# Performance work log

Hardware: AMD Instinct MI355X
Metric: run time of the kernel (lower is better)

The kernel has to match this reference:

```python
import jax, jax.numpy as jnp
import numpy as np

B, S, D, H = 4, 2048, 1024, 16
DH = D // H  # 64
EPS = 1e-5


def setup_inputs() -> dict:
    key = jax.random.key(0)
    ks = jax.random.split(key, 6)
    scale = 0.02
    return {
        "x": jax.random.normal(ks[0], (B, S, D), dtype=jnp.float32),
        "Wq": jax.random.normal(ks[1], (H, D, DH), dtype=jnp.float32) * scale,
        "Wk": jax.random.normal(ks[2], (H, D, DH), dtype=jnp.float32) * scale,
        "Wv": jax.random.normal(ks[3], (H, D, DH), dtype=jnp.float32) * scale,
        "Wo": jax.random.normal(ks[4], (D, D), dtype=jnp.float32) * scale,
        "bo": jnp.zeros((D,), dtype=jnp.float32),
        "gamma": jnp.ones((D,), dtype=jnp.float32),
        "beta": jnp.zeros((D,), dtype=jnp.float32),
    }


def reference(x, Wq, Wk, Wv, Wo, bo, gamma, beta):
    # Per-head projections, stacked across heads: [B,H,S,DH]
    q = jnp.einsum("bsd,hdk->bhsk", x, Wq)
    k = jnp.einsum("bsd,hdk->bhsk", x, Wk)
    v = jnp.einsum("bsd,hdk->bhsk", x, Wv)
    inv_scale = 1.0 / jnp.sqrt(jnp.float32(DH))  # key.size(-1) == head_dim
    scores = jnp.einsum("bhqk,bhsk->bhqs", q, k) * inv_scale  # [B,H,S,S]
    attn = jax.nn.softmax(scores, axis=-1)
    ctx = jnp.einsum("bhqs,bhsk->bhqk", attn, v)  # [B,H,S,DH]
    # concat heads -> [B,S,D]
    concat = jnp.transpose(ctx, (0, 2, 1, 3)).reshape(B, S, D)
    proj = concat @ Wo + bo  # fc_out (Wo stored as [in,out])
    added = proj + x  # residual add
    mu = jnp.mean(added, axis=-1, keepdims=True)
    var = jnp.mean(jnp.square(added - mu), axis=-1, keepdims=True)
    normed = (added - mu) * jax.lax.rsqrt(var + EPS)
    return normed * gamma + beta
```

## Files before the change

### kernel.cpp

```cpp
#include <hip/hip_runtime.h>
#include <hip/hip_bf16.h>
#include <stdint.h>

#define DEV __device__ __forceinline__

typedef short s16x8 __attribute__((ext_vector_type(8)));
typedef float f32x4 __attribute__((ext_vector_type(4)));

DEV void async_load16(const void* g, void* l) {
  __builtin_amdgcn_global_load_lds((void __attribute__((address_space(1)))*)(g),
                                   (void __attribute__((address_space(3)))*)(l),
                                   16, 0, 0);
}

__global__ __launch_bounds__(256) void cast_x_kernel(const float* __restrict__ in,
                                                     __hip_bfloat16* __restrict__ out, int n4) {
  int i = blockIdx.x * 256 + threadIdx.x;
  if (i >= n4) return;
  float4 v = ((const float4*)in)[i];
  alignas(8) __hip_bfloat16 t[4] = {__float2bfloat16(v.x), __float2bfloat16(v.y),
                                    __float2bfloat16(v.z), __float2bfloat16(v.w)};
  *(uint2*)(out + (size_t)i * 4) = *(const uint2*)t;
}

__global__ __launch_bounds__(256) void transpose_cast_kernel(const float* __restrict__ src,
                                                             __hip_bfloat16* __restrict__ dst,
                                                             int R, int C, float scale) {
  __shared__ float tile[64][65];
  const int r0 = blockIdx.x * 64, c0 = blockIdx.y * 64, bt = blockIdx.z;
  const int tc = threadIdx.x & 63, tr = threadIdx.x >> 6;
  const float* sp = src + (size_t)bt * R * C;
#pragma unroll
  for (int rr = 0; rr < 64; rr += 4)
    tile[tr + rr][tc] = sp[(size_t)(r0 + tr + rr) * C + c0 + tc];
  __syncthreads();
  __hip_bfloat16* dp = dst + (size_t)bt * R * C;
#pragma unroll
  for (int rr = 0; rr < 64; rr += 4) {
    int cc = tr + rr;
    dp[(size_t)(c0 + cc) * R + r0 + tc] = __float2bfloat16(tile[tc][cc] * scale);
  }
}

template <int MODE>
__global__ __launch_bounds__(256) void gemm128(const __hip_bfloat16* __restrict__ A,
                                               const __hip_bfloat16* __restrict__ Bt,
                                               void* __restrict__ out0,
                                               void* __restrict__ out1,
                                               const float* __restrict__ bias,
                                               const float* __restrict__ resid,
                                               int M, int N, int K) {
  __shared__ __hip_bfloat16 As[128 * 32];
  __shared__ __hip_bfloat16 Bs[128 * 32];
  const int tid = threadIdx.x;
  const int lane = tid & 63, w = tid >> 6;
  const int lr = lane & 15, lq = lane >> 4;
  const int wm = w >> 1, wn = w & 1;
  const int m0 = blockIdx.y * 128, n0 = blockIdx.x * 128;

  const f32x4 fz = {0.f, 0.f, 0.f, 0.f};
  f32x4 acc[4][4];
#pragma unroll
  for (int i = 0; i < 4; i++)
#pragma unroll
    for (int j = 0; j < 4; j++) acc[i][j] = fz;

  const int kiters = K >> 5;
  for (int kt = 0; kt < kiters; kt++) {
    __syncthreads();
#pragma unroll
    for (int r = 0; r < 2; r++) {
      const int c = r * 256 + tid;
      const int row = c >> 2, kc = c & 3;
      async_load16((const short*)A + (size_t)(m0 + row) * K + kt * 32 + kc * 8,
                   (char*)As + (r * 256 + (tid & 0xC0)) * 16);
      async_load16((const short*)Bt + (size_t)(n0 + row) * K + kt * 32 + kc * 8,
                   (char*)Bs + (r * 256 + (tid & 0xC0)) * 16);
    }
    __syncthreads();
    const short* Ap = (const short*)As;
    const short* Bp = (const short*)Bs;
    s16x8 av[4], bv[4];
#pragma unroll
    for (int i = 0; i < 4; i++)
      av[i] = *(const s16x8*)(Ap + (wm * 64 + i * 16 + lr) * 32 + lq * 8);
#pragma unroll
    for (int j = 0; j < 4; j++)
      bv[j] = *(const s16x8*)(Bp + (wn * 64 + j * 16 + lr) * 32 + lq * 8);
#pragma unroll
    for (int i = 0; i < 4; i++)
#pragma unroll
      for (int j = 0; j < 4; j++)
        acc[i][j] = __builtin_amdgcn_mfma_f32_16x16x32_bf16(av[i], bv[j], acc[i][j], 0, 0, 0);
  }

  __hip_bfloat16* dst01 = nullptr;
  if constexpr (MODE == 0) dst01 = (__hip_bfloat16*)((n0 < 1024) ? out0 : out1);

#pragma unroll
  for (int i = 0; i < 4; i++)
#pragma unroll
    for (int j = 0; j < 4; j++)
#pragma unroll
      for (int r = 0; r < 4; r++) {
        const int row = m0 + wm * 64 + i * 16 + lq * 4 + r;
        const int col = n0 + wn * 64 + j * 16 + lr;
        const float v = acc[i][j][r];
        if constexpr (MODE == 0) {
          const int bb = row >> 11, s = row & 2047;
          const int colq = col & 1023;
          dst01[((((size_t)bb * 16 + (colq >> 6)) * 2048 + s) << 6) + (col & 63)] =
              __float2bfloat16(v);
        } else if constexpr (MODE == 1) {
          const int bb = col >> 11, s = col & 2047;
          ((__hip_bfloat16*)out0)[(size_t)bb * 2097152 + (size_t)row * 2048 + s] =
              __float2bfloat16(v);
        } else {
          const size_t idx = (size_t)row * 1024 + col;
          ((float*)out0)[idx] = v + bias[col] + resid[idx];
        }
      }
}

__global__ __launch_bounds__(256, 4) void flash_kernel(const __hip_bfloat16* __restrict__ Qg,
                                                       const __hip_bfloat16* __restrict__ Kg,
                                                       const __hip_bfloat16* __restrict__ Vtg,
                                                       __hip_bfloat16* __restrict__ Og) {
  __shared__ __hip_bfloat16 Klds[128 * 64];
  __shared__ __hip_bfloat16 Vlds[64 * 128];
  __shared__ __hip_bfloat16 Plds[64 * 64];
  const int tid = threadIdx.x;
  const int lane = tid & 63, w = tid >> 6;
  const int lr = lane & 15, lq = lane >> 4;
  const int qt = blockIdx.x, h = blockIdx.y, b = blockIdx.z;
  const size_t bh = (size_t)b * 16 + h;
  const short* Qbase = (const short*)Qg + (bh * 2048 + (size_t)qt * 128) * 64;
  const short* Kbh = (const short*)Kg + bh * 2048 * 64;
  const short* Vbh = (const short*)Vtg + bh * 64 * 2048;

  s16x8 qb[2][2];
#pragma unroll
  for (int nt = 0; nt < 2; nt++)
#pragma unroll
    for (int ks = 0; ks < 2; ks++)
      qb[nt][ks] = *(const s16x8*)(Qbase + (w * 32 + nt * 16 + lr) * 64 + ks * 32 + lq * 8);

  const f32x4 fz = {0.f, 0.f, 0.f, 0.f};
  f32x4 o[2][4];
#pragma unroll
  for (int mt = 0; mt < 2; mt++)
#pragma unroll
    for (int nt = 0; nt < 4; nt++) o[mt][nt] = fz;
  float lsum[2] = {0.f, 0.f};

  for (int kb = 0; kb < 16; kb++) {
    __syncthreads();
    const short* Ksrc = Kbh + kb * 128 * 64;
#pragma unroll
    for (int r = 0; r < 4; r++) {
      int c = r * 256 + tid;
      int row = c >> 3, ck = c & 7;
      async_load16(Ksrc + row * 64 + (ck ^ (row & 7)) * 8,
                   (char*)Klds + (r * 256 + (tid & 0xC0)) * 16);
    }
#pragma unroll
    for (int r = 0; r < 4; r++) {
      int c = r * 256 + tid;
      int row = c >> 4, ck = c & 15;
      async_load16(Vbh + (size_t)row * 2048 + kb * 128 + (ck ^ (row & 15)) * 8,
                   (char*)Vlds + (r * 256 + (tid & 0xC0)) * 16);
    }
    __syncthreads();

    const short* Kp = (const short*)Klds;
    const short* Vp = (const short*)Vlds;
    short* Pp = (short*)Plds;

#pragma unroll
    for (int c = 0; c < 4; c++) {
      s16x8 kf[2][2];
#pragma unroll
      for (int mt = 0; mt < 2; mt++)
#pragma unroll
        for (int ks = 0; ks < 2; ks++) {
          int kvrow = c * 32 + mt * 16 + lr;
          kf[mt][ks] = *(const s16x8*)(Kp + kvrow * 64 + ((ks * 4 + lq) ^ (kvrow & 7)) * 8);
        }
      f32x4 st[2][2];
#pragma unroll
      for (int mt = 0; mt < 2; mt++)
#pragma unroll
        for (int nt = 0; nt < 2; nt++) st[mt][nt] = fz;
#pragma unroll
      for (int mt = 0; mt < 2; mt++)
#pragma unroll
        for (int ks = 0; ks < 2; ks++)
#pragma unroll
          for (int nt = 0; nt < 2; nt++)
            st[mt][nt] =
                __builtin_amdgcn_mfma_f32_16x16x32_bf16(kf[mt][ks], qb[nt][ks], st[mt][nt], 0, 0, 0);

#pragma unroll
      for (int mt = 0; mt < 2; mt++)
#pragma unroll
        for (int nt = 0; nt < 2; nt++) {
          float e0 = __expf(st[mt][nt][0]);
          float e1 = __expf(st[mt][nt][1]);
          float e2 = __expf(st[mt][nt][2]);
          float e3 = __expf(st[mt][nt][3]);
          lsum[nt] += (e0 + e1) + (e2 + e3);
          int q = w * 32 + nt * 16 + lr;
          int p = q >> 1, u = q & 1;
          int lineChunk = u * 4 + mt * 2 + (lq >> 1);
          int addr = p * 64 + ((lineChunk ^ (p & 7)) << 3) + (lq & 1) * 4;
          alignas(8) __hip_bfloat16 t4[4] = {__float2bfloat16(e0), __float2bfloat16(e1),
                                             __float2bfloat16(e2), __float2bfloat16(e3)};
          *(uint2*)(Pp + addr) = *(const uint2*)t4;
        }

      s16x8 pa[2];
#pragma unroll
      for (int mt = 0; mt < 2; mt++) {
        int q = w * 32 + mt * 16 + lr;
        int p = q >> 1, u = q & 1;
        pa[mt] = *(const s16x8*)(Pp + p * 64 + (((u * 4 + lq) ^ (p & 7)) << 3));
      }
#pragma unroll
      for (int nt = 0; nt < 4; nt++) {
        int vrow = nt * 16 + lr;
        s16x8 vb = *(const s16x8*)(Vp + vrow * 128 + (((c * 4 + lq) ^ (vrow & 15)) << 3));
        o[0][nt] = __builtin_amdgcn_mfma_f32_16x16x32_bf16(pa[0], vb, o[0][nt], 0, 0, 0);
        o[1][nt] = __builtin_amdgcn_mfma_f32_16x16x32_bf16(pa[1], vb, o[1][nt], 0, 0, 0);
      }
    }
  }

#pragma unroll
  for (int nt = 0; nt < 2; nt++) {
    lsum[nt] += __shfl_xor(lsum[nt], 16);
    lsum[nt] += __shfl_xor(lsum[nt], 32);
  }

#pragma unroll
  for (int mt = 0; mt < 2; mt++)
#pragma unroll
    for (int r = 0; r < 4; r++) {
      float lv = __shfl(lsum[mt], lq * 4 + r);
      float inv = 1.0f / lv;
      int rowg = qt * 128 + w * 32 + mt * 16 + lq * 4 + r;
#pragma unroll
      for (int nt = 0; nt < 4; nt++) {
        Og[((size_t)b * 2048 + rowg) * 1024 + h * 64 + nt * 16 + lr] =
            __float2bfloat16(o[mt][nt][r] * inv);
      }
    }
}

__global__ __launch_bounds__(256) void ln_kernel(const float* __restrict__ tmp,
                                                 const float* __restrict__ gamma,
                                                 const float* __restrict__ beta,
                                                 float* __restrict__ out) {
  const int row = blockIdx.x, tid = threadIdx.x;
  const int lane = tid & 63, w = tid >> 6;
  const float* rp = tmp + (size_t)row * 1024;
  float4 v = ((const float4*)rp)[tid];
  float s = v.x + v.y + v.z + v.w;
  float ss = v.x * v.x + v.y * v.y + v.z * v.z + v.w * v.w;
#pragma unroll
  for (int off = 32; off >= 1; off >>= 1) {
    s += __shfl_xor(s, off);
    ss += __shfl_xor(ss, off);
  }
  __shared__ float red[8];
  if (lane == 0) {
    red[w] = s;
    red[4 + w] = ss;
  }
  __syncthreads();
  s = red[0] + red[1] + red[2] + red[3];
  ss = red[4] + red[5] + red[6] + red[7];
  const float mu = s * (1.0f / 1024.0f);
  const float var = ss * (1.0f / 1024.0f) - mu * mu;
  const float rstd = rsqrtf(var + 1e-5f);
  float4 g = ((const float4*)gamma)[tid];
  float4 be = ((const float4*)beta)[tid];
  float4 ov;
  ov.x = (v.x - mu) * rstd * g.x + be.x;
  ov.y = (v.y - mu) * rstd * g.y + be.y;
  ov.z = (v.z - mu) * rstd * g.z + be.z;
  ov.w = (v.w - mu) * rstd * g.w + be.w;
  ((float4*)(out + (size_t)row * 1024))[tid] = ov;
}

extern "C" void kernel_launch(void* const* d_in, const int* in_sizes, int n_in,
                              void* d_out, int out_size, void* d_ws, size_t ws_size,
                              hipStream_t stream) {
  (void)in_sizes; (void)n_in; (void)out_size; (void)ws_size;
  const float* x = (const float*)d_in[0];
  const float* Wq = (const float*)d_in[1];
  const float* Wk = (const float*)d_in[2];
  const float* Wv = (const float*)d_in[3];
  const float* Wo = (const float*)d_in[4];
  const float* bo = (const float*)d_in[5];
  const float* gamma = (const float*)d_in[6];
  const float* beta = (const float*)d_in[7];
  float* out = (float*)d_out;
  char* ws = (char*)d_ws;

  __hip_bfloat16* xb = (__hip_bfloat16*)(ws + 0);
  __hip_bfloat16* wqT = (__hip_bfloat16*)(ws + 16777216);
  __hip_bfloat16* wkT = (__hip_bfloat16*)(ws + 18874368);
  __hip_bfloat16* wvT = (__hip_bfloat16*)(ws + 20971520);
  __hip_bfloat16* woT = (__hip_bfloat16*)(ws + 23068672);
  __hip_bfloat16* Q = (__hip_bfloat16*)(ws + 25165824);
  __hip_bfloat16* Kt = (__hip_bfloat16*)(ws + 41943040);
  __hip_bfloat16* Vt = (__hip_bfloat16*)(ws + 58720256);
  __hip_bfloat16* cc = (__hip_bfloat16*)(ws + 75497472);
  float* tmp = (float*)(ws + 25165824);

  cast_x_kernel<<<8192, 256, 0, stream>>>(x, xb, 2097152);
  transpose_cast_kernel<<<dim3(16, 1, 16), 256, 0, stream>>>(Wq, wqT, 1024, 64, 0.125f);
  transpose_cast_kernel<<<dim3(16, 1, 16), 256, 0, stream>>>(Wk, wkT, 1024, 64, 1.0f);
  transpose_cast_kernel<<<dim3(16, 1, 16), 256, 0, stream>>>(Wv, wvT, 1024, 64, 1.0f);
  transpose_cast_kernel<<<dim3(16, 16, 1), 256, 0, stream>>>(Wo, woT, 1024, 1024, 1.0f);

  gemm128<0><<<dim3(16, 64), 256, 0, stream>>>(xb, wqT, Q, Kt, nullptr, nullptr, 8192, 2048, 1024);
  gemm128<1><<<dim3(64, 8), 256, 0, stream>>>(wvT, xb, Vt, nullptr, nullptr, nullptr, 1024, 8192, 1024);

  flash_kernel<<<dim3(16, 16, 4), 256, 0, stream>>>(Q, Kt, Vt, cc);

  gemm128<2><<<dim3(8, 64), 256, 0, stream>>>(cc, woT, tmp, nullptr, bo, x, 8192, 1024, 1024);
  ln_kernel<<<8192, 256, 0, stream>>>(tmp, gamma, beta, out);
}
```

Before: 330.8 us.

## Keep softmax probabilities in registers and enlarge flash query tile to 256

The flash kernel now builds the P operand directly in registers. It permutes the K rows so the score MFMA output layout matches the A-operand layout of the PV MFMA, which removes the LDS round trip for P. Each block now covers 256 query rows (64 per wave), halving K/V loads per query, and the grid is reordered so the head/batch index varies fastest. The log2(e) factor is folded into the Q weight scale so exp2 and rcp intrinsics replace expf and division. The cost is roughly doubled accumulator registers, which drops occupancy to 2 blocks per CU, and a grid of only 512 blocks.

```diff
diff --git a/kernel.cpp b/kernel.cpp
--- a/kernel.cpp
+++ b/kernel.cpp
@@ -6,11 +6,19 @@
 
 typedef short s16x8 __attribute__((ext_vector_type(8)));
 typedef float f32x4 __attribute__((ext_vector_type(4)));
+typedef int i32x4 __attribute__((ext_vector_type(4)));
 
 DEV void async_load16(const void* g, void* l) {
   __builtin_amdgcn_global_load_lds((void __attribute__((address_space(1)))*)(g),
                                    (void __attribute__((address_space(3)))*)(l),
                                    16, 0, 0);
+}
+
+DEV unsigned pack_bf16x2(float a, float b) {
+  __hip_bfloat162 h = __float22bfloat162_rn(make_float2(a, b));
+  union { __hip_bfloat162 h2; unsigned u; } cv;
+  cv.h2 = h;
+  return cv.u;
 }
 
 __global__ __launch_bounds__(256) void cast_x_kernel(const float* __restrict__ in,
@@ -122,36 +130,39 @@
       }
 }
 
-__global__ __launch_bounds__(256, 4) void flash_kernel(const __hip_bfloat16* __restrict__ Qg,
+__global__ __launch_bounds__(256, 2) void flash_kernel(const __hip_bfloat16* __restrict__ Qg,
                                                        const __hip_bfloat16* __restrict__ Kg,
                                                        const __hip_bfloat16* __restrict__ Vtg,
                                                        __hip_bfloat16* __restrict__ Og) {
   __shared__ __hip_bfloat16 Klds[128 * 64];
   __shared__ __hip_bfloat16 Vlds[64 * 128];
-  __shared__ __hip_bfloat16 Plds[64 * 64];
   const int tid = threadIdx.x;
   const int lane = tid & 63, w = tid >> 6;
   const int lr = lane & 15, lq = lane >> 4;
-  const int qt = blockIdx.x, h = blockIdx.y, b = blockIdx.z;
+  const int hb = blockIdx.x, qt = blockIdx.y;
+  const int h = hb >> 2, b = hb & 3;
   const size_t bh = (size_t)b * 16 + h;
-  const short* Qbase = (const short*)Qg + (bh * 2048 + (size_t)qt * 128) * 64;
+  const short* Qbase = (const short*)Qg + (bh * 2048 + (size_t)qt * 256) * 64;
   const short* Kbh = (const short*)Kg + bh * 2048 * 64;
   const short* Vbh = (const short*)Vtg + bh * 64 * 2048;
 
-  s16x8 qb[2][2];
-#pragma unroll
-  for (int nt = 0; nt < 2; nt++)
+  const int rbase = (lr >> 2) * 8 + (lr & 3);
+  const int gk = (lr & 3) | (((lr >> 2) & 1) << 2);
+
+  s16x8 qb[4][2];
+#pragma unroll
+  for (int nt = 0; nt < 4; nt++)
 #pragma unroll
     for (int ks = 0; ks < 2; ks++)
-      qb[nt][ks] = *(const s16x8*)(Qbase + (w * 32 + nt * 16 + lr) * 64 + ks * 32 + lq * 8);
+      qb[nt][ks] = *(const s16x8*)(Qbase + (w * 64 + nt * 16 + lr) * 64 + ks * 32 + lq * 8);
 
   const f32x4 fz = {0.f, 0.f, 0.f, 0.f};
-  f32x4 o[2][4];
-#pragma unroll
-  for (int mt = 0; mt < 2; mt++)
-#pragma unroll
-    for (int nt = 0; nt < 4; nt++) o[mt][nt] = fz;
-  float lsum[2] = {0.f, 0.f};
+  f32x4 o[4][4];
+#pragma unroll
+  for (int i = 0; i < 4; i++)
+#pragma unroll
+    for (int j = 0; j < 4; j++) o[i][j] = fz;
+  float lsum[4] = {0.f, 0.f, 0.f, 0.f};
 
   for (int kb = 0; kb < 16; kb++) {
     __syncthreads();
@@ -160,7 +171,8 @@
     for (int r = 0; r < 4; r++) {
       int c = r * 256 + tid;
       int row = c >> 3, ck = c & 7;
-      async_load16(Ksrc + row * 64 + (ck ^ (row & 7)) * 8,
+      int g = (row & 3) | (((row >> 3) & 1) << 2);
+      async_load16(Ksrc + row * 64 + (ck ^ g) * 8,
                    (char*)Klds + (r * 256 + (tid & 0xC0)) * 16);
     }
 #pragma unroll
@@ -174,84 +186,59 @@
 
     const short* Kp = (const short*)Klds;
     const short* Vp = (const short*)Vlds;
-    short* Pp = (short*)Plds;
 
 #pragma unroll
     for (int c = 0; c < 4; c++) {
-      s16x8 kf[2][2];
-#pragma unroll
-      for (int mt = 0; mt < 2; mt++)
-#pragma unroll
-        for (int ks = 0; ks < 2; ks++) {
-          int kvrow = c * 32 + mt * 16 + lr;
-          kf[mt][ks] = *(const s16x8*)(Kp + kvrow * 64 + ((ks * 4 + lq) ^ (kvrow & 7)) * 8);
+      union { i32x4 i; s16x8 s; } pa[4];
+
+#pragma unroll
+      for (int mt = 0; mt < 2; mt++) {
+        const int kvrow = c * 32 + mt * 4 + rbase;
+        s16x8 kf0 = *(const s16x8*)(Kp + kvrow * 64 + ((0 * 4 + lq) ^ gk) * 8);
+        s16x8 kf1 = *(const s16x8*)(Kp + kvrow * 64 + ((1 * 4 + lq) ^ gk) * 8);
+#pragma unroll
+        for (int nt = 0; nt < 4; nt++) {
+          f32x4 st = fz;
+          st = __builtin_amdgcn_mfma_f32_16x16x32_bf16(kf0, qb[nt][0], st, 0, 0, 0);
+          st = __builtin_amdgcn_mfma_f32_16x16x32_bf16(kf1, qb[nt][1], st, 0, 0, 0);
+          float e0 = __builtin_amdgcn_exp2f(st[0]);
+          float e1 = __builtin_amdgcn_exp2f(st[1]);
+          float e2 = __builtin_amdgcn_exp2f(st[2]);
+          float e3 = __builtin_amdgcn_exp2f(st[3]);
+          lsum[nt] += (e0 + e1) + (e2 + e3);
+          pa[nt].i[mt * 2 + 0] = (int)pack_bf16x2(e0, e1);
+          pa[nt].i[mt * 2 + 1] = (int)pack_bf16x2(e2, e3);
         }
-      f32x4 st[2][2];
-#pragma unroll
-      for (int mt = 0; mt < 2; mt++)
-#pragma unroll
-        for (int nt = 0; nt < 2; nt++) st[mt][nt] = fz;
-#pragma unroll
-      for (int mt = 0; mt < 2; mt++)
-#pragma unroll
-        for (int ks = 0; ks < 2; ks++)
-#pragma unroll
-          for (int nt = 0; nt < 2; nt++)
-            st[mt][nt] =
-                __builtin_amdgcn_mfma_f32_16x16x32_bf16(kf[mt][ks], qb[nt][ks], st[mt][nt], 0, 0, 0);
-
-#pragma unroll
-      for (int mt = 0; mt < 2; mt++)
-#pragma unroll
-        for (int nt = 0; nt < 2; nt++) {
-          float e0 = __expf(st[mt][nt][0]);
-          float e1 = __expf(st[mt][nt][1]);
-          float e2 = __expf(st[mt][nt][2]);
-          float e3 = __expf(st[mt][nt][3]);
-          lsum[nt] += (e0 + e1) + (e2 + e3);
-          int q = w * 32 + nt * 16 + lr;
-          int p = q >> 1, u = q & 1;
-          int lineChunk = u * 4 + mt * 2 + (lq >> 1);
-          int addr = p * 64 + ((lineChunk ^ (p & 7)) << 3) + (lq & 1) * 4;
-          alignas(8) __hip_bfloat16 t4[4] = {__float2bfloat16(e0), __float2bfloat16(e1),
-                                             __float2bfloat16(e2), __float2bfloat16(e3)};
-          *(uint2*)(Pp + addr) = *(const uint2*)t4;
-        }
-
-      s16x8 pa[2];
-#pragma unroll
-      for (int mt = 0; mt < 2; mt++) {
-        int q = w * 32 + mt * 16 + lr;
-        int p = q >> 1, u = q & 1;
-        pa[mt] = *(const s16x8*)(Pp + p * 64 + (((u * 4 + lq) ^ (p & 7)) << 3));
       }
-#pragma unroll
-      for (int nt = 0; nt < 4; nt++) {
-        int vrow = nt * 16 + lr;
-        s16x8 vb = *(const s16x8*)(Vp + vrow * 128 + (((c * 4 + lq) ^ (vrow & 15)) << 3));
-        o[0][nt] = __builtin_amdgcn_mfma_f32_16x16x32_bf16(pa[0], vb, o[0][nt], 0, 0, 0);
-        o[1][nt] = __builtin_amdgcn_mfma_f32_16x16x32_bf16(pa[1], vb, o[1][nt], 0, 0, 0);
+
+#pragma unroll
+      for (int ndh = 0; ndh < 4; ndh++) {
+        int vrow = ndh * 16 + lr;
+        s16x8 vb = *(const s16x8*)(Vp + vrow * 128 + (((c * 4 + lq) ^ lr) << 3));
+#pragma unroll
+        for (int nt = 0; nt < 4; nt++)
+          o[nt][ndh] = __builtin_amdgcn_mfma_f32_16x16x32_bf16(pa[nt].s, vb, o[nt][ndh], 0, 0, 0);
       }
     }
   }
 
 #pragma unroll
-  for (int nt = 0; nt < 2; nt++) {
+  for (int nt = 0; nt < 4; nt++) {
     lsum[nt] += __shfl_xor(lsum[nt], 16);
     lsum[nt] += __shfl_xor(lsum[nt], 32);
   }
 
 #pragma unroll
-  for (int mt = 0; mt < 2; mt++)
+  for (int nt = 0; nt < 4; nt++)
 #pragma unroll
     for (int r = 0; r < 4; r++) {
-      float lv = __shfl(lsum[mt], lq * 4 + r);
-      float inv = 1.0f / lv;
-      int rowg = qt * 128 + w * 32 + mt * 16 + lq * 4 + r;
-#pragma unroll
-      for (int nt = 0; nt < 4; nt++) {
-        Og[((size_t)b * 2048 + rowg) * 1024 + h * 64 + nt * 16 + lr] =
-            __float2bfloat16(o[mt][nt][r] * inv);
+      float lv = __shfl(lsum[nt], lq * 4 + r);
+      float inv = __builtin_amdgcn_rcpf(lv);
+      int rowg = qt * 256 + w * 64 + nt * 16 + lq * 4 + r;
+#pragma unroll
+      for (int ndh = 0; ndh < 4; ndh++) {
+        Og[((size_t)b * 2048 + rowg) * 1024 + h * 64 + ndh * 16 + lr] =
+            __float2bfloat16(o[nt][ndh][r] * inv);
       }
     }
 }
@@ -319,7 +306,8 @@
   float* tmp = (float*)(ws + 25165824);
 
   cast_x_kernel<<<8192, 256, 0, stream>>>(x, xb, 2097152);
-  transpose_cast_kernel<<<dim3(16, 1, 16), 256, 0, stream>>>(Wq, wqT, 1024, 64, 0.125f);
+  transpose_cast_kernel<<<dim3(16, 1, 16), 256, 0, stream>>>(Wq, wqT, 1024, 64,
+                                                             0.125f * 1.44269504088896f);
   transpose_cast_kernel<<<dim3(16, 1, 16), 256, 0, stream>>>(Wk, wkT, 1024, 64, 1.0f);
   transpose_cast_kernel<<<dim3(16, 1, 16), 256, 0, stream>>>(Wv, wvT, 1024, 64, 1.0f);
   transpose_cast_kernel<<<dim3(16, 16, 1), 256, 0, stream>>>(Wo, woT, 1024, 1024, 1.0f);
@@ -327,7 +315,7 @@
   gemm128<0><<<dim3(16, 64), 256, 0, stream>>>(xb, wqT, Q, Kt, nullptr, nullptr, 8192, 2048, 1024);
   gemm128<1><<<dim3(64, 8), 256, 0, stream>>>(wvT, xb, Vt, nullptr, nullptr, nullptr, 1024, 8192, 1024);
 
-  flash_kernel<<<dim3(16, 16, 4), 256, 0, stream>>>(Q, Kt, Vt, cc);
+  flash_kernel<<<dim3(64, 8), 256, 0, stream>>>(Q, Kt, Vt, cc);
 
   gemm128<2><<<dim3(8, 64), 256, 0, stream>>>(cc, woT, tmp, nullptr, bo, x, 8192, 1024, 1024);
   ln_kernel<<<8192, 256, 0, stream>>>(tmp, gamma, beta, out);
```

New measurement: 326.5 us. About the same (-1.3%).
